# Kernel tuning notes

Measured on AMD Instinct MI355X. Metric: run time of the kernel, lower is better.

Reference implementation:

```python
import math
import jax, jax.numpy as jnp
import numpy as np

B, T, C = 4, 2048, 1024
H = 16
D = C // H  # head_dim = 64


def setup_inputs() -> dict:
    key = jax.random.key(0)
    ks = jax.random.split(key, 5)
    scale = 0.02
    return {
        "x": jax.random.normal(ks[0], (B, T, C), dtype=jnp.float32),
        "w_attn": jax.random.normal(ks[1], (C, 3 * C), dtype=jnp.float32) * scale,
        "b_attn": jax.random.normal(ks[2], (3 * C,), dtype=jnp.float32) * scale,
        "w_proj": jax.random.normal(ks[3], (C, C), dtype=jnp.float32) * scale,
        "b_proj": jax.random.normal(ks[4], (C,), dtype=jnp.float32) * scale,
    }


def reference(x, w_attn, b_attn, w_proj, b_proj):
    b, t, c = x.shape
    qkv = x @ w_attn + b_attn                       # [B,T,3C]
    q, k, v = jnp.split(qkv, 3, axis=-1)
    q = q.reshape(b, t, H, D)
    k = k.reshape(b, t, H, D)
    v = v.reshape(b, t, H, D)
    # scores: [B,H,T,T]
    att = jnp.einsum('bthd,bshd->bhts', q, k) * (1.0 / math.sqrt(D))
    causal = jnp.tril(jnp.ones((t, t), dtype=bool))
    att = jnp.where(causal, att, -jnp.inf)
    att = jax.nn.softmax(att, axis=-1)
    y = jnp.einsum('bhts,bshd->bthd', att, v).reshape(b, t, c)
    return y @ w_proj + b_proj
```

## Files before the change

### kernel.cpp

```cpp
#include <hip/hip_runtime.h>

#define BB 4
#define TT 2048
#define CC 1024
#define HH 16
#define DD 64
#define MM (BB*TT)
#define N3 (3*CC)
#define NTK 16
#define QSCL 0.18033688011112043f

typedef unsigned short u16;
typedef __attribute__((ext_vector_type(8))) __bf16 bf16x8;
typedef __attribute__((ext_vector_type(4))) float f32x4;
typedef __attribute__((ext_vector_type(8))) u16 u16x8;
typedef __attribute__((ext_vector_type(4))) u16 u16x4;

__device__ __forceinline__ u16 f2bf(float f) {
  return __builtin_bit_cast(u16, (__bf16)f);
}

__device__ __forceinline__ void gload16(const void* g, void* lds) {
  __builtin_amdgcn_global_load_lds(
      (const __attribute__((address_space(1))) void*)g,
      (__attribute__((address_space(3))) void*)lds, 16, 0, 0);
}

__global__ __launch_bounds__(256) void k_prep(const float* __restrict__ x,
                                              const float* __restrict__ wa, const float* __restrict__ wp,
                                              u16* __restrict__ Xb,
                                              u16* __restrict__ WaT, u16* __restrict__ WpT) {
  __shared__ float t[32][33];
  int bid = blockIdx.x;
  int tid = threadIdx.x;
  if (bid < 4096) {
    size_t i = ((size_t)bid * 256 + tid) * 8;
    f32x4 a = *(const f32x4*)(x + i);
    f32x4 b = *(const f32x4*)(x + i + 4);
    u16x8 o;
    o[0]=f2bf(a[0]); o[1]=f2bf(a[1]); o[2]=f2bf(a[2]); o[3]=f2bf(a[3]);
    o[4]=f2bf(b[0]); o[5]=f2bf(b[1]); o[6]=f2bf(b[2]); o[7]=f2bf(b[3]);
    *(u16x8*)(Xb + i) = o;
  } else {
    int t2 = bid - 4096;
    int gx = t2 & 127;
    int rb = (t2 >> 7) * 32;
    const float* in; u16* out; int Cc, cb;
    if (gx < 96) { in = wa; out = WaT; Cc = N3; cb = gx * 32; }
    else         { in = wp; out = WpT; Cc = CC; cb = (gx - 96) * 32; }
    int tx = tid & 31, ty = tid >> 5;
    #pragma unroll
    for (int j = 0; j < 4; ++j)
      t[ty + j*8][tx] = in[(size_t)(rb + ty + j*8) * Cc + cb + tx];
    __syncthreads();
    #pragma unroll
    for (int j = 0; j < 4; ++j)
      out[(size_t)(cb + ty + j*8) * CC + rb + tx] = f2bf(t[tx][ty + j*8]);
  }
}

__device__ __forceinline__ void gemm_ring(const u16* __restrict__ A, const u16* __restrict__ Bt,
                                          int mbase, int nbase,
                                          u16 (*As)[128*64], u16 (*Bs)[256*64],
                                          f32x4 acc[4][4]) {
  int tid = threadIdx.x;
  int lane = tid & 63;
  int wid = tid >> 6;
  int wm = (wid >> 2) * 64, wn = (wid & 3) * 64;
  int r = lane & 15, g = lane >> 4;

  auto STAGE_A = [&](int sl, int u) {
    int kb = u * 64;
    #pragma unroll
    for (int i = 0; i < 2; ++i) {
      int c = tid + 512*i;
      int row = c >> 3, ch = c & 7;
      int chs = ch ^ (row & 7);
      gload16(A + (size_t)(mbase + row)*CC + kb + chs*8, &As[sl][c*8]);
    }
  };
  auto STAGE_B1 = [&](int sl, int u, int i) {
    int kb = u * 64;
    int c = tid + 512*i;
    int row = c >> 3, ch = c & 7;
    int chs = ch ^ (row & 7);
    gload16(Bt + (size_t)(nbase + row)*CC + kb + chs*8, &Bs[sl][c*8]);
  };

  STAGE_A(0, 0); STAGE_B1(0, 0, 0); STAGE_B1(0, 0, 1); STAGE_B1(0, 0, 2); STAGE_B1(0, 0, 3);
  STAGE_A(1, 1); STAGE_B1(1, 1, 0); STAGE_B1(1, 1, 1); STAGE_B1(1, 1, 2); STAGE_B1(1, 1, 3);
  asm volatile("s_waitcnt vmcnt(6)" ::: "memory");
  __builtin_amdgcn_s_barrier();

  int sl = 0;
  for (int u = 0; u < NTK; ++u) {
    int s2 = sl + 2; if (s2 >= 3) s2 -= 3;
    bool pre = (u + 2 < NTK);
    #pragma unroll
    for (int ks = 0; ks < 2; ++ks) {
      bf16x8 af[4], bfr[4];
      #pragma unroll
      for (int mi = 0; mi < 4; ++mi)
        af[mi]  = *(const bf16x8*)&As[sl][(wm + mi*16 + r)*64 + (((ks*4 + g) ^ (r & 7)) << 3)];
      #pragma unroll
      for (int ni = 0; ni < 4; ++ni)
        bfr[ni] = *(const bf16x8*)&Bs[sl][(wn + ni*16 + r)*64 + (((ks*4 + g) ^ (r & 7)) << 3)];
      if (pre) {
        if (ks == 0) { STAGE_A(s2, u + 2); STAGE_B1(s2, u + 2, 0); }
        else         { STAGE_B1(s2, u + 2, 1); STAGE_B1(s2, u + 2, 2); STAGE_B1(s2, u + 2, 3); }
      }
      __builtin_amdgcn_s_barrier();
      __builtin_amdgcn_s_setprio(1);
      #pragma unroll
      for (int mi = 0; mi < 4; ++mi)
        #pragma unroll
        for (int ni = 0; ni < 4; ++ni)
          acc[mi][ni] = __builtin_amdgcn_mfma_f32_16x16x32_bf16(af[mi], bfr[ni], acc[mi][ni], 0, 0, 0);
      __builtin_amdgcn_s_setprio(0);
      if (ks == 1) {
        if (pre) asm volatile("s_waitcnt vmcnt(6)" ::: "memory");
        else     asm volatile("s_waitcnt vmcnt(0)" ::: "memory");
      }
      __builtin_amdgcn_s_barrier();
    }
    ++sl; if (sl >= 3) sl -= 3;
  }
}

__device__ __forceinline__ void grid_map(int bid, int& bx, int& by) {
  int xcd = bid & 7;
  int idx = bid >> 3;
  bx = xcd * 8 + (idx & 7);
  by = idx >> 3;
}

__global__ __launch_bounds__(512) void k_gemm_qkv(const u16* __restrict__ Xb, const u16* __restrict__ WaT,
                                                  const float* __restrict__ b_attn,
                                                  u16* __restrict__ Qh, u16* __restrict__ Kh,
                                                  u16* __restrict__ Vt) {
  __shared__ u16 As[3][128*64];
  __shared__ u16 Bs[3][256*64];
  f32x4 acc[4][4] = {};
  int bx, by; grid_map(blockIdx.x, bx, by);
  int mbase = bx * 128, nbase = by * 256;
  gemm_ring(Xb, WaT, mbase, nbase, As, Bs, acc);
  int lane = threadIdx.x & 63, wid = threadIdx.x >> 6;
  int wm = (wid >> 2) * 64, wn = (wid & 3) * 64;
  int r = lane & 15, g = lane >> 4;
  int which = nbase >> 10;
  if (which < 2) {
    u16* dst = which == 0 ? Qh : Kh;
    float scl = which == 0 ? QSCL : 1.0f;
    #pragma unroll
    for (int mi = 0; mi < 4; ++mi)
      #pragma unroll
      for (int ni = 0; ni < 4; ++ni)
        #pragma unroll
        for (int reg = 0; reg < 4; ++reg) {
          int m = mbase + wm + mi*16 + 4*g + reg;
          int n = nbase + wn + ni*16 + r;
          float v = (acc[mi][ni][reg] + b_attn[n]) * scl;
          int ccol = n & (CC - 1);
          int h = ccol >> 6, d = ccol & 63;
          int bb = m >> 11, t = m & (TT - 1);
          dst[((size_t)(bb*HH + h)*TT + t)*DD + d] = f2bf(v);
        }
  } else {
    #pragma unroll
    for (int mi = 0; mi < 4; ++mi)
      #pragma unroll
      for (int ni = 0; ni < 4; ++ni) {
        int m0 = mbase + wm + mi*16 + 4*g;
        int n = nbase + wn + ni*16 + r;
        float bn = b_attn[n];
        int ccol = n & (CC - 1);
        int h = ccol >> 6, d = ccol & 63;
        int bb = m0 >> 11, t0 = m0 & (TT - 1);
        u16x4 pk;
        #pragma unroll
        for (int reg = 0; reg < 4; ++reg)
          pk[reg] = f2bf(acc[mi][ni][reg] + bn);
        *(u16x4*)&Vt[((size_t)(bb*HH + h)*DD + d)*TT + t0] = pk;
      }
  }
}

__global__ __launch_bounds__(512) void k_gemm_proj(const u16* __restrict__ Yh, const u16* __restrict__ WpT,
                                                   const float* __restrict__ b_proj,
                                                   float* __restrict__ out) {
  __shared__ u16 As[3][128*64];
  __shared__ u16 Bs[3][256*64];
  f32x4 acc[4][4] = {};
  int bx, by; grid_map(blockIdx.x, bx, by);
  int mbase = bx * 128, nbase = by * 256;
  gemm_ring(Yh, WpT, mbase, nbase, As, Bs, acc);
  int lane = threadIdx.x & 63, wid = threadIdx.x >> 6;
  int wm = (wid >> 2) * 64, wn = (wid & 3) * 64;
  int r = lane & 15, g = lane >> 4;
  #pragma unroll
  for (int mi = 0; mi < 4; ++mi)
    #pragma unroll
    for (int ni = 0; ni < 4; ++ni)
      #pragma unroll
      for (int reg = 0; reg < 4; ++reg) {
        int m = mbase + wm + mi*16 + 4*g + reg;
        int n = nbase + wn + ni*16 + r;
        out[(size_t)m*CC + n] = acc[mi][ni][reg] + b_proj[n];
      }
}

__global__ __launch_bounds__(256) void k_attn(const u16* __restrict__ Qh, const u16* __restrict__ Kh,
                                              const u16* __restrict__ Vtg, u16* __restrict__ Yh) {
  __shared__ u16 Ks[2][128*64];
  __shared__ u16 Vs[2][64*128];
  __shared__ u16 Pl[4][32*64];
  int bid = blockIdx.x;
  int bh = (bid & 7) * 8 + (bid >> 6);
  int p  = (bid >> 3) & 7;
  int b = bh >> 4, h = bh & 15;
  int tid = threadIdx.x, lane = tid & 63, w = tid >> 6;
  int r = lane & 15, g = lane >> 4;
  size_t hoff = (size_t)bh * TT * DD;
  u16* pw = Pl[w];

  bf16x8 ones;
  #pragma unroll
  for (int e = 0; e < 8; ++e) ones[e] = (__bf16)1.0f;

  int koff[4], voff[4], kld[4], vld[4];
  #pragma unroll
  for (int i = 0; i < 4; ++i) {
    int c = tid + 256*i;
    int krow = c >> 3, kch = c & 7;
    koff[i] = krow*DD + (kch ^ (krow & 7))*8;
    int vrow = c >> 4, vch = c & 15;
    voff[i] = vrow*TT + ((vch ^ (vrow & 7)))*8;
    kld[i] = c*8; vld[i] = c*8;
  }
  const u16* Kg0 = Kh  + hoff;
  const u16* Vg0 = Vtg + hoff;

  auto STAGE = [&](int bsel, int kb) {
    const u16* kbase = Kg0 + (size_t)kb * (128*DD);
    const u16* vbase = Vg0 + (size_t)kb * 128;
    u16* Kd = bsel ? &Ks[1][0] : &Ks[0][0];
    u16* Vd = bsel ? &Vs[1][0] : &Vs[0][0];
    #pragma unroll
    for (int i = 0; i < 4; ++i) gload16(kbase + koff[i], Kd + kld[i]);
    #pragma unroll
    for (int i = 0; i < 4; ++i) gload16(vbase + voff[i], Vd + vld[i]);
  };

  for (int ph = 0; ph < 2; ++ph) {
    int qt = ph == 0 ? (15 - p) : p;
    int qrow0 = qt*128 + w*32;
    int nkb = qt + 1;

    bf16x8 qf[2][2];
    #pragma unroll
    for (int ni = 0; ni < 2; ++ni)
      #pragma unroll
      for (int ks = 0; ks < 2; ++ks)
        qf[ni][ks] = *(const bf16x8*)(Qh + hoff + (size_t)(qrow0 + ni*16 + r)*DD + ks*32 + g*8);

    f32x4 o[2][4] = {};
    f32x4 lacc[2] = {};

    STAGE(0, 0);
    __syncthreads();
    int buf = 0;

    for (int kb = 0; kb < nkb; ++kb) {
      if (kb + 1 < nkb) STAGE(buf ^ 1, kb + 1);

      #pragma unroll
      for (int kc = 0; kc < 2; ++kc) {
        int keybase = kb*128 + kc*64;
        if (keybase <= qrow0 + 31) {
          f32x4 s[2][4] = {};
          __builtin_amdgcn_s_setprio(1);
          #pragma unroll
          for (int nf = 0; nf < 4; ++nf)
            #pragma unroll
            for (int ks = 0; ks < 2; ++ks) {
              bf16x8 kf = *(const bf16x8*)&Ks[buf][(kc*64 + nf*16 + r)*64 + (((ks*4 + g) ^ (r & 7)) << 3)];
              #pragma unroll
              for (int ni = 0; ni < 2; ++ni)
                s[ni][nf] = __builtin_amdgcn_mfma_f32_16x16x32_bf16(kf, qf[ni][ks], s[ni][nf], 0, 0, 0);
            }
          __builtin_amdgcn_s_setprio(0);
          bool need_mask = (keybase + 63 > qrow0);
          if (need_mask) {
            #pragma unroll
            for (int ni = 0; ni < 2; ++ni)
              #pragma unroll
              for (int nf = 0; nf < 4; ++nf)
                #pragma unroll
                for (int reg = 0; reg < 4; ++reg) {
                  int key = keybase + nf*16 + 4*g + reg;
                  int qrow = qrow0 + ni*16 + r;
                  float sv = (key > qrow) ? -1e30f : s[ni][nf][reg];
                  s[ni][nf][reg] = __builtin_amdgcn_exp2f(sv);
                }
          } else {
            #pragma unroll
            for (int ni = 0; ni < 2; ++ni)
              #pragma unroll
              for (int nf = 0; nf < 4; ++nf)
                #pragma unroll
                for (int reg = 0; reg < 4; ++reg)
                  s[ni][nf][reg] = __builtin_amdgcn_exp2f(s[ni][nf][reg]);
          }
          #pragma unroll
          for (int ni = 0; ni < 2; ++ni)
            #pragma unroll
            for (int nf = 0; nf < 4; ++nf) {
              int qh_ = ni*16 + r;
              int chunk = 2*nf + (g >> 1);
              u16x4 pk;
              #pragma unroll
              for (int reg = 0; reg < 4; ++reg) pk[reg] = f2bf(s[ni][nf][reg]);
              *(u16x4*)&pw[qh_*64 + ((chunk ^ (qh_ & 7)) << 3) + ((g & 1) << 2)] = pk;
            }
          __builtin_amdgcn_s_setprio(1);
          #pragma unroll
          for (int ks = 0; ks < 2; ++ks) {
            bf16x8 pb[2];
            #pragma unroll
            for (int ni = 0; ni < 2; ++ni)
              pb[ni] = *(const bf16x8*)&pw[(ni*16 + r)*64 + (((ks*4 + g) ^ (r & 7)) << 3)];
            #pragma unroll
            for (int nf2 = 0; nf2 < 4; ++nf2) {
              bf16x8 vf = *(const bf16x8*)&Vs[buf][(nf2*16 + r)*128 + (((kc*8 + ks*4 + g) ^ (r & 7)) << 3)];
              #pragma unroll
              for (int ni = 0; ni < 2; ++ni)
                o[ni][nf2] = __builtin_amdgcn_mfma_f32_16x16x32_bf16(vf, pb[ni], o[ni][nf2], 0, 0, 0);
            }
            #pragma unroll
            for (int ni = 0; ni < 2; ++ni)
              lacc[ni] = __builtin_amdgcn_mfma_f32_16x16x32_bf16(ones, pb[ni], lacc[ni], 0, 0, 0);
          }
          __builtin_amdgcn_s_setprio(0);
        }
      }
      __syncthreads();
      buf ^= 1;
    }

    #pragma unroll
    for (int ni = 0; ni < 2; ++ni) {
      float inv = 1.0f / lacc[ni][0];
      int t = qrow0 + ni*16 + r;
      #pragma unroll
      for (int nf2 = 0; nf2 < 4; ++nf2) {
        u16x4 pk;
        #pragma unroll
        for (int reg = 0; reg < 4; ++reg)
          pk[reg] = f2bf(o[ni][nf2][reg] * inv);
        *(u16x4*)&Yh[((size_t)b*TT + t)*CC + h*DD + nf2*16 + 4*g] = pk;
      }
    }
  }
}

extern "C" void kernel_launch(void* const* d_in, const int* in_sizes, int n_in,
                              void* d_out, int out_size, void* d_ws, size_t ws_size,
                              hipStream_t stream) {
  const float* x      = (const float*)d_in[0];
  const float* w_attn = (const float*)d_in[1];
  const float* b_attn = (const float*)d_in[2];
  const float* w_proj = (const float*)d_in[3];
  const float* b_proj = (const float*)d_in[4];
  float* out = (float*)d_out;

  u16* Xb  = (u16*)d_ws;
  u16* WaT = Xb  + (size_t)MM*CC;
  u16* WpT = WaT + (size_t)N3*CC;
  u16* Qh  = WpT + (size_t)CC*CC;
  u16* Kh  = Qh  + (size_t)BB*HH*TT*DD;
  u16* Vt  = Kh  + (size_t)BB*HH*TT*DD;
  u16* Yh  = Vt  + (size_t)BB*HH*TT*DD;

  k_prep<<<dim3(8192), dim3(256), 0, stream>>>(x, w_attn, w_proj, Xb, WaT, WpT);
  k_gemm_qkv<<<dim3((MM/128)*(N3/256)), dim3(512), 0, stream>>>(Xb, WaT, b_attn, Qh, Kh, Vt);
  k_attn<<<dim3(BB*HH*8), dim3(256), 0, stream>>>(Qh, Kh, Vt, Yh);
  k_gemm_proj<<<dim3((MM/128)*(CC/256)), dim3(512), 0, stream>>>(Yh, WpT, b_proj, out);
}
```

Before: 155.1 us.

## Process paired high and low query tiles in one shared KV sweep

Previously each block handled two query tiles (15-p and p) in two separate phases, and each phase streamed its own K/V blocks. Now both tiles keep their Q fragments and accumulators live at once and share a single pass over the K/V blocks, so the low tile reuses the staged K/V of the early blocks. This removes the second round of global-to-LDS loads and its barriers. The cost is roughly double the accumulator registers, which may lower occupancy or cause spills.

```diff
diff --git a/kernel.cpp b/kernel.cpp
--- a/kernel.cpp
+++ b/kernel.cpp
@@ -251,114 +251,123 @@
     for (int i = 0; i < 4; ++i) gload16(vbase + voff[i], Vd + vld[i]);
   };
 
-  for (int ph = 0; ph < 2; ++ph) {
-    int qt = ph == 0 ? (15 - p) : p;
-    int qrow0 = qt*128 + w*32;
-    int nkb = qt + 1;
-
-    bf16x8 qf[2][2];
+  int qtH = 15 - p, qtL = p;
+  int qrow0H = qtH*128 + w*32, qrow0L = qtL*128 + w*32;
+  int nkb = qtH + 1;
+
+  bf16x8 qfH[2][2], qfL[2][2];
+  #pragma unroll
+  for (int ni = 0; ni < 2; ++ni)
+    #pragma unroll
+    for (int ks = 0; ks < 2; ++ks) {
+      qfH[ni][ks] = *(const bf16x8*)(Qh + hoff + (size_t)(qrow0H + ni*16 + r)*DD + ks*32 + g*8);
+      qfL[ni][ks] = *(const bf16x8*)(Qh + hoff + (size_t)(qrow0L + ni*16 + r)*DD + ks*32 + g*8);
+    }
+
+  f32x4 oH[2][4] = {}, oL[2][4] = {};
+  f32x4 laccH[2] = {}, laccL[2] = {};
+
+  auto TILE = [&](int qrow0, bf16x8 (&qf)[2][2], f32x4 (&o)[2][4], f32x4 (&lacc)[2],
+                  int keybase, int kc, int buf) {
+    f32x4 s[2][4] = {};
+    __builtin_amdgcn_s_setprio(1);
+    #pragma unroll
+    for (int nf = 0; nf < 4; ++nf)
+      #pragma unroll
+      for (int ks = 0; ks < 2; ++ks) {
+        bf16x8 kf = *(const bf16x8*)&Ks[buf][(kc*64 + nf*16 + r)*64 + (((ks*4 + g) ^ (r & 7)) << 3)];
+        #pragma unroll
+        for (int ni = 0; ni < 2; ++ni)
+          s[ni][nf] = __builtin_amdgcn_mfma_f32_16x16x32_bf16(kf, qf[ni][ks], s[ni][nf], 0, 0, 0);
+      }
+    __builtin_amdgcn_s_setprio(0);
+    bool need_mask = (keybase + 63 > qrow0);
+    if (need_mask) {
+      #pragma unroll
+      for (int ni = 0; ni < 2; ++ni)
+        #pragma unroll
+        for (int nf = 0; nf < 4; ++nf)
+          #pragma unroll
+          for (int reg = 0; reg < 4; ++reg) {
+            int key = keybase + nf*16 + 4*g + reg;
+            int qrow = qrow0 + ni*16 + r;
+            float sv = (key > qrow) ? -1e30f : s[ni][nf][reg];
+            s[ni][nf][reg] = __builtin_amdgcn_exp2f(sv);
+          }
+    } else {
+      #pragma unroll
+      for (int ni = 0; ni < 2; ++ni)
+        #pragma unroll
+        for (int nf = 0; nf < 4; ++nf)
+          #pragma unroll
+          for (int reg = 0; reg < 4; ++reg)
+            s[ni][nf][reg] = __builtin_amdgcn_exp2f(s[ni][nf][reg]);
+    }
     #pragma unroll
     for (int ni = 0; ni < 2; ++ni)
       #pragma unroll
-      for (int ks = 0; ks < 2; ++ks)
-        qf[ni][ks] = *(const bf16x8*)(Qh + hoff + (size_t)(qrow0 + ni*16 + r)*DD + ks*32 + g*8);
-
-    f32x4 o[2][4] = {};
-    f32x4 lacc[2] = {};
-
-    STAGE(0, 0);
+      for (int nf = 0; nf < 4; ++nf) {
+        int qh_ = ni*16 + r;
+        int chunk = 2*nf + (g >> 1);
+        u16x4 pk;
+        #pragma unroll
+        for (int reg = 0; reg < 4; ++reg) pk[reg] = f2bf(s[ni][nf][reg]);
+        *(u16x4*)&pw[qh_*64 + ((chunk ^ (qh_ & 7)) << 3) + ((g & 1) << 2)] = pk;
+      }
+    __builtin_amdgcn_s_setprio(1);
+    #pragma unroll
+    for (int ks = 0; ks < 2; ++ks) {
+      bf16x8 pb[2];
+      #pragma unroll
+      for (int ni = 0; ni < 2; ++ni)
+        pb[ni] = *(const bf16x8*)&pw[(ni*16 + r)*64 + (((ks*4 + g) ^ (r & 7)) << 3)];
+      #pragma unroll
+      for (int nf2 = 0; nf2 < 4; ++nf2) {
+        bf16x8 vf = *(const bf16x8*)&Vs[buf][(nf2*16 + r)*128 + (((kc*8 + ks*4 + g) ^ (r & 7)) << 3)];
+        #pragma unroll
+        for (int ni = 0; ni < 2; ++ni)
+          o[ni][nf2] = __builtin_amdgcn_mfma_f32_16x16x32_bf16(vf, pb[ni], o[ni][nf2], 0, 0, 0);
+      }
+      #pragma unroll
+      for (int ni = 0; ni < 2; ++ni)
+        lacc[ni] = __builtin_amdgcn_mfma_f32_16x16x32_bf16(ones, pb[ni], lacc[ni], 0, 0, 0);
+    }
+    __builtin_amdgcn_s_setprio(0);
+  };
+
+  STAGE(0, 0);
+  __syncthreads();
+  int buf = 0;
+
+  for (int kb = 0; kb < nkb; ++kb) {
+    if (kb + 1 < nkb) STAGE(buf ^ 1, kb + 1);
+
+    #pragma unroll
+    for (int kc = 0; kc < 2; ++kc) {
+      int keybase = kb*128 + kc*64;
+      if (keybase <= qrow0H + 31) TILE(qrow0H, qfH, oH, laccH, keybase, kc, buf);
+      if (keybase <= qrow0L + 31) TILE(qrow0L, qfL, oL, laccL, keybase, kc, buf);
+    }
     __syncthreads();
-    int buf = 0;
-
-    for (int kb = 0; kb < nkb; ++kb) {
-      if (kb + 1 < nkb) STAGE(buf ^ 1, kb + 1);
-
-      #pragma unroll
-      for (int kc = 0; kc < 2; ++kc) {
-        int keybase = kb*128 + kc*64;
-        if (keybase <= qrow0 + 31) {
-          f32x4 s[2][4] = {};
-          __builtin_amdgcn_s_setprio(1);
-          #pragma unroll
-          for (int nf = 0; nf < 4; ++nf)
-            #pragma unroll
-            for (int ks = 0; ks < 2; ++ks) {
-              bf16x8 kf = *(const bf16x8*)&Ks[buf][(kc*64 + nf*16 + r)*64 + (((ks*4 + g) ^ (r & 7)) << 3)];
-              #pragma unroll
-              for (int ni = 0; ni < 2; ++ni)
-                s[ni][nf] = __builtin_amdgcn_mfma_f32_16x16x32_bf16(kf, qf[ni][ks], s[ni][nf], 0, 0, 0);
-            }
-          __builtin_amdgcn_s_setprio(0);
-          bool need_mask = (keybase + 63 > qrow0);
-          if (need_mask) {
-            #pragma unroll
-            for (int ni = 0; ni < 2; ++ni)
-              #pragma unroll
-              for (int nf = 0; nf < 4; ++nf)
-                #pragma unroll
-                for (int reg = 0; reg < 4; ++reg) {
-                  int key = keybase + nf*16 + 4*g + reg;
-                  int qrow = qrow0 + ni*16 + r;
-                  float sv = (key > qrow) ? -1e30f : s[ni][nf][reg];
-                  s[ni][nf][reg] = __builtin_amdgcn_exp2f(sv);
-                }
-          } else {
-            #pragma unroll
-            for (int ni = 0; ni < 2; ++ni)
-              #pragma unroll
-              for (int nf = 0; nf < 4; ++nf)
-                #pragma unroll
-                for (int reg = 0; reg < 4; ++reg)
-                  s[ni][nf][reg] = __builtin_amdgcn_exp2f(s[ni][nf][reg]);
-          }
-          #pragma unroll
-          for (int ni = 0; ni < 2; ++ni)
-            #pragma unroll
-            for (int nf = 0; nf < 4; ++nf) {
-              int qh_ = ni*16 + r;
-              int chunk = 2*nf + (g >> 1);
-              u16x4 pk;
-              #pragma unroll
-              for (int reg = 0; reg < 4; ++reg) pk[reg] = f2bf(s[ni][nf][reg]);
-              *(u16x4*)&pw[qh_*64 + ((chunk ^ (qh_ & 7)) << 3) + ((g & 1) << 2)] = pk;
-            }
-          __builtin_amdgcn_s_setprio(1);
-          #pragma unroll
-          for (int ks = 0; ks < 2; ++ks) {
-            bf16x8 pb[2];
-            #pragma unroll
-            for (int ni = 0; ni < 2; ++ni)
-              pb[ni] = *(const bf16x8*)&pw[(ni*16 + r)*64 + (((ks*4 + g) ^ (r & 7)) << 3)];
-            #pragma unroll
-            for (int nf2 = 0; nf2 < 4; ++nf2) {
-              bf16x8 vf = *(const bf16x8*)&Vs[buf][(nf2*16 + r)*128 + (((kc*8 + ks*4 + g) ^ (r & 7)) << 3)];
-              #pragma unroll
-              for (int ni = 0; ni < 2; ++ni)
-                o[ni][nf2] = __builtin_amdgcn_mfma_f32_16x16x32_bf16(vf, pb[ni], o[ni][nf2], 0, 0, 0);
-            }
-            #pragma unroll
-            for (int ni = 0; ni < 2; ++ni)
-              lacc[ni] = __builtin_amdgcn_mfma_f32_16x16x32_bf16(ones, pb[ni], lacc[ni], 0, 0, 0);
-          }
-          __builtin_amdgcn_s_setprio(0);
-        }
-      }
-      __syncthreads();
-      buf ^= 1;
-    }
-
-    #pragma unroll
-    for (int ni = 0; ni < 2; ++ni) {
-      float inv = 1.0f / lacc[ni][0];
-      int t = qrow0 + ni*16 + r;
-      #pragma unroll
-      for (int nf2 = 0; nf2 < 4; ++nf2) {
-        u16x4 pk;
-        #pragma unroll
-        for (int reg = 0; reg < 4; ++reg)
-          pk[reg] = f2bf(o[ni][nf2][reg] * inv);
-        *(u16x4*)&Yh[((size_t)b*TT + t)*CC + h*DD + nf2*16 + 4*g] = pk;
-      }
+    buf ^= 1;
+  }
+
+  #pragma unroll
+  for (int ni = 0; ni < 2; ++ni) {
+    float invH = 1.0f / laccH[ni][0];
+    float invL = 1.0f / laccL[ni][0];
+    int tH = qrow0H + ni*16 + r;
+    int tL = qrow0L + ni*16 + r;
+    #pragma unroll
+    for (int nf2 = 0; nf2 < 4; ++nf2) {
+      u16x4 pkH, pkL;
+      #pragma unroll
+      for (int reg = 0; reg < 4; ++reg) {
+        pkH[reg] = f2bf(oH[ni][nf2][reg] * invH);
+        pkL[reg] = f2bf(oL[ni][nf2][reg] * invL);
+      }
+      *(u16x4*)&Yh[((size_t)b*TT + tH)*CC + h*DD + nf2*16 + 4*g] = pkH;
+      *(u16x4*)&Yh[((size_t)b*TT + tL)*CC + h*DD + nf2*16 + 4*g] = pkL;
     }
   }
 }
```

Result: slower. 176.1 us (+13.5%).
